# Optimization experiments

Hardware: AMD Instinct MI355X
Metric: run time of the kernel (lower is better)

## Reference

```python
import jax, jax.numpy as jnp
import numpy as np

N_USER = 50000
N_ITEM = 50000
N_EDGE = 1600000
D_IN = 64
D_OUT = 64


def _mean_agg(msgs, dst, num_dst):
    # copy_u + mean: segment-mean of edge messages onto dst nodes; zero for
    # zero-in-degree nodes (DGL default).
    s = jax.ops.segment_sum(msgs, dst, num_segments=num_dst)          # [Nd, D]
    cnt = jax.ops.segment_sum(jnp.ones((msgs.shape[0],), msgs.dtype), dst,
                              num_segments=num_dst)                    # [Nd]
    return s / jnp.maximum(cnt, 1.0)[:, None]


def setup_inputs() -> dict:
    key = jax.random.key(0)
    ks = jax.random.split(key, 12)
    return {
        'user_feat': jax.random.normal(ks[0], (N_USER, D_IN), jnp.float32),
        'item_feat': jax.random.normal(ks[1], (N_ITEM, D_IN), jnp.float32),
        'rate_src': jax.random.randint(ks[2], (N_EDGE,), 0, N_USER, jnp.int64 if jax.config.jax_enable_x64 else jnp.int32),
        'rate_dst': jax.random.randint(ks[3], (N_EDGE,), 0, N_ITEM, jnp.int64 if jax.config.jax_enable_x64 else jnp.int32),
        'rev_src': jax.random.randint(ks[4], (N_EDGE,), 0, N_ITEM, jnp.int64 if jax.config.jax_enable_x64 else jnp.int32),
        'rev_dst': jax.random.randint(ks[5], (N_EDGE,), 0, N_USER, jnp.int64 if jax.config.jax_enable_x64 else jnp.int32),
        'W_rate': jax.random.normal(ks[6], (D_IN, D_OUT), jnp.float32) * (1.0 / np.sqrt(D_IN)),
        'b_rate': jnp.zeros((D_OUT,), jnp.float32),
        'W_rev': jax.random.normal(ks[7], (D_IN, D_OUT), jnp.float32) * (1.0 / np.sqrt(D_IN)),
        'b_rev': jnp.zeros((D_OUT,), jnp.float32),
        'loop_weight': jax.random.normal(ks[8], (D_IN, D_OUT), jnp.float32) * (1.0 / np.sqrt(D_IN)),
        'h_bias': jnp.zeros((D_OUT,), jnp.float32),
    }


def reference(user_feat, item_feat, rate_src, rate_dst, rev_src, rev_dst,
              W_rate, b_rate, W_rev, b_rev, loop_weight, h_bias):
    # Per-etype Linear on source-node features (applied node-wise, as in torch).
    Wh_rate = user_feat @ W_rate + b_rate      # [Nu, Dout], etype 'rate': user->item
    Wh_rev = item_feat @ W_rev + b_rev         # [Ni, Dout], etype 'rated-by': item->user

    # copy_u + mean per etype, cross-reduce 'sum' (one etype per dst ntype here).
    h_item = _mean_agg(Wh_rate[rate_src], rate_dst, N_ITEM)
    h_user = _mean_agg(Wh_rev[rev_src], rev_dst, N_USER)

    # self-loop + bias (dropout p=0.0 is identity)
    h_user = h_user + user_feat @ loop_weight + h_bias
    h_item = h_item + item_feat @ loop_weight + h_bias
    return (h_user, h_item)
```

## Files before the change

### kernel.cpp

```cpp
#include <hip/hip_runtime.h>

#define N_USER 50000
#define N_ITEM 50000
#define N_NODE 50000
#define N_EDGE 1600000
#define D 64

#define FB_SHIFT 7
#define N_FINE 400
#define CAP 5120
#define BIN_CHUNK 2048
#define NCAST 3125
#define NBIN ((N_EDGE + BIN_CHUNK - 1) / BIN_CHUNK)

typedef __attribute__((ext_vector_type(8))) short short8;
typedef __attribute__((ext_vector_type(4))) float floatx4;

__device__ __forceinline__ unsigned short f32_to_bf16(float x) {
    unsigned u = __float_as_uint(x);
    unsigned r = (u + 0x7FFFu + ((u >> 16) & 1u)) >> 16;
    return (unsigned short)r;
}
__device__ __forceinline__ float bf16_to_f32(unsigned short h) {
    return __uint_as_float(((unsigned)h) << 16);
}

__global__ __launch_bounds__(256) void cast_bin(
    const float4* __restrict__ fU, ushort4* __restrict__ bU,
    const float4* __restrict__ fI, ushort4* __restrict__ bI,
    const int* __restrict__ srcA, const int* __restrict__ dstA, unsigned* __restrict__ binA,
    const int* __restrict__ srcB, const int* __restrict__ dstB, unsigned* __restrict__ binB,
    int* __restrict__ fcur)
{
    __shared__ int hist[N_FINE];
    __shared__ int lcur[N_FINE];
    const int id = blockIdx.x;

    if (id >= 2 * NBIN) {
        const int cid = id - 2 * NBIN;
        const int et = (cid >= NCAST) ? 1 : 0;
        const float4* __restrict__ in = et ? fI : fU;
        ushort4* __restrict__ out     = et ? bI : bU;
        int i = (cid - et * NCAST) * 256 + threadIdx.x;
        float4 v = in[i];
        ushort4 o;
        o.x = f32_to_bf16(v.x); o.y = f32_to_bf16(v.y);
        o.z = f32_to_bf16(v.z); o.w = f32_to_bf16(v.w);
        out[i] = o;
        return;
    }

    const int et = (id >= NBIN) ? 1 : 0;
    const int chunk = id - et * NBIN;
    const int* __restrict__ src = et ? srcB : srcA;
    const int* __restrict__ dst = et ? dstB : dstA;
    unsigned* __restrict__ bin  = et ? binB : binA;
    int* __restrict__ fc = fcur + et * N_FINE;

    for (int i = threadIdx.x; i < N_FINE; i += 256) hist[i] = 0;
    __syncthreads();

    const int base = chunk * BIN_CHUNK;
    const int n4 = (min(BIN_CHUNK, N_EDGE - base)) >> 2;
    const int4* dst4 = (const int4*)(dst + base);
    const int4* src4 = (const int4*)(src + base);

    for (int i = threadIdx.x; i < n4; i += 256) {
        int4 d = dst4[i];
        atomicAdd(&hist[d.x >> FB_SHIFT], 1);
        atomicAdd(&hist[d.y >> FB_SHIFT], 1);
        atomicAdd(&hist[d.z >> FB_SHIFT], 1);
        atomicAdd(&hist[d.w >> FB_SHIFT], 1);
    }
    __syncthreads();
    for (int f = threadIdx.x; f < N_FINE; f += 256) {
        int c = hist[f];
        lcur[f] = c ? (f * CAP + atomicAdd(&fc[f], c)) : 0;
    }
    __syncthreads();
    for (int i = threadIdx.x; i < n4; i += 256) {
        int4 d = dst4[i];
        int4 s = src4[i];
        { int pos = atomicAdd(&lcur[d.x >> FB_SHIFT], 1); bin[pos] = ((unsigned)d.x << 16) | (unsigned)s.x; }
        { int pos = atomicAdd(&lcur[d.y >> FB_SHIFT], 1); bin[pos] = ((unsigned)d.y << 16) | (unsigned)s.y; }
        { int pos = atomicAdd(&lcur[d.z >> FB_SHIFT], 1); bin[pos] = ((unsigned)d.z << 16) | (unsigned)s.z; }
        { int pos = atomicAdd(&lcur[d.w >> FB_SHIFT], 1); bin[pos] = ((unsigned)d.w << 16) | (unsigned)s.w; }
    }
}

__global__ __launch_bounds__(256) void bucket_sort(
    const unsigned* __restrict__ binI, unsigned short* __restrict__ srtI,
    int* __restrict__ offI, int* __restrict__ cntI,
    const unsigned* __restrict__ binU, unsigned short* __restrict__ srtU,
    int* __restrict__ offU, int* __restrict__ cntU,
    const int* __restrict__ fcur)
{
    const int et = blockIdx.y;
    const unsigned* __restrict__ bin = et ? binU : binI;
    unsigned short* __restrict__ srt = et ? srtU : srtI;
    int* __restrict__ off  = et ? offU : offI;
    int* __restrict__ cntG = et ? cntU : cntI;
    const int f = blockIdx.x;
    const int start = f * CAP;
    const int end   = start + fcur[et * N_FINE + f];
    const int nodebase = f << FB_SHIFT;

    __shared__ int cnt[128];
    __shared__ int sc[128];
    __shared__ int pos[128];
    if (threadIdx.x < 128) cnt[threadIdx.x] = 0;
    __syncthreads();

    for (int e = start + threadIdx.x; e < end; e += 256) {
        int ld = (int)(bin[e] >> 16) - nodebase;
        atomicAdd(&cnt[ld], 1);
    }
    __syncthreads();

    if (threadIdx.x < 128) sc[threadIdx.x] = cnt[threadIdx.x];
    __syncthreads();
    for (int o = 1; o < 128; o <<= 1) {
        int t = 0;
        if (threadIdx.x < 128 && threadIdx.x >= o) t = sc[threadIdx.x - o];
        __syncthreads();
        if (threadIdx.x < 128) sc[threadIdx.x] += t;
        __syncthreads();
    }
    if (threadIdx.x < 128) {
        int base = start + sc[threadIdx.x] - cnt[threadIdx.x];
        pos[threadIdx.x] = base;
        int node = nodebase + threadIdx.x;
        if (node < N_NODE) { off[node] = base; cntG[node] = cnt[threadIdx.x]; }
    }
    __syncthreads();

    for (int e = start + threadIdx.x; e < end; e += 256) {
        unsigned p = bin[e];
        int ld = (int)(p >> 16) - nodebase;
        int q = atomicAdd(&pos[ld], 1);
        srt[q] = (unsigned short)(p & 0xFFFFu);
    }
}

__global__ __launch_bounds__(256) void aggregate_kernel(
    const ushort4* __restrict__ itemB,
    const ushort4* __restrict__ userB,
    const int* __restrict__ offU, const int* __restrict__ cntU, const unsigned short* __restrict__ srtU,
    const int* __restrict__ offI, const int* __restrict__ cntI, const unsigned short* __restrict__ srtI,
    ushort4* __restrict__ aggU, ushort4* __restrict__ aggI)
{
    int g = blockIdx.x * 16 + (threadIdx.x >> 4);
    if (g >= N_USER + N_ITEM) return;
    const int lane = threadIdx.x & 15;

    const bool isUser = (g < N_USER);
    const int d = isUser ? g : g - N_USER;
    const ushort4* __restrict__ tab = isUser ? itemB : userB;
    const int* __restrict__ off     = isUser ? offU : offI;
    const int* __restrict__ cntG    = isUser ? cntU : cntI;
    const unsigned short* __restrict__ srt = isUser ? srtU : srtI;
    ushort4* __restrict__ agg       = isUser ? aggU : aggI;

    const int start = off[d];
    const int c     = cntG[d];
    const int end   = start + c;

    float4 a0 = make_float4(0.f, 0.f, 0.f, 0.f);
    float4 a1 = make_float4(0.f, 0.f, 0.f, 0.f);
    float4 a2 = make_float4(0.f, 0.f, 0.f, 0.f);
    float4 a3 = make_float4(0.f, 0.f, 0.f, 0.f);
    int e = start;
    for (; e + 4 <= end; e += 4) {
        int s0 = (int)srt[e],     s1 = (int)srt[e + 1];
        int s2 = (int)srt[e + 2], s3 = (int)srt[e + 3];
        ushort4 w0 = tab[(size_t)s0 * 16 + lane];
        ushort4 w1 = tab[(size_t)s1 * 16 + lane];
        ushort4 w2 = tab[(size_t)s2 * 16 + lane];
        ushort4 w3 = tab[(size_t)s3 * 16 + lane];
        a0.x += bf16_to_f32(w0.x); a0.y += bf16_to_f32(w0.y);
        a0.z += bf16_to_f32(w0.z); a0.w += bf16_to_f32(w0.w);
        a1.x += bf16_to_f32(w1.x); a1.y += bf16_to_f32(w1.y);
        a1.z += bf16_to_f32(w1.z); a1.w += bf16_to_f32(w1.w);
        a2.x += bf16_to_f32(w2.x); a2.y += bf16_to_f32(w2.y);
        a2.z += bf16_to_f32(w2.z); a2.w += bf16_to_f32(w2.w);
        a3.x += bf16_to_f32(w3.x); a3.y += bf16_to_f32(w3.y);
        a3.z += bf16_to_f32(w3.z); a3.w += bf16_to_f32(w3.w);
    }
    for (; e < end; ++e) {
        int s0 = (int)srt[e];
        ushort4 w0 = tab[(size_t)s0 * 16 + lane];
        a0.x += bf16_to_f32(w0.x); a0.y += bf16_to_f32(w0.y);
        a0.z += bf16_to_f32(w0.z); a0.w += bf16_to_f32(w0.w);
    }
    a0.x += a1.x + a2.x + a3.x;
    a0.y += a1.y + a2.y + a3.y;
    a0.z += a1.z + a2.z + a3.z;
    a0.w += a1.w + a2.w + a3.w;

    const float inv = (c > 0) ? 1.0f / (float)c : 0.0f;
    ushort4 o;
    o.x = f32_to_bf16(a0.x * inv);
    o.y = f32_to_bf16(a0.y * inv);
    o.z = f32_to_bf16(a0.z * inv);
    o.w = f32_to_bf16(a0.w * inv);
    agg[(size_t)g * 16 + lane - (isUser ? 0 : (size_t)N_USER * 16)] = o;
}

__global__ __launch_bounds__(256, 4) void final_gemm(
    const unsigned short* __restrict__ aggU_, const unsigned short* __restrict__ featU_,
    const int* __restrict__ cntU_, const float* __restrict__ WU,
    const float* __restrict__ beU,
    const unsigned short* __restrict__ aggI_, const unsigned short* __restrict__ featI_,
    const int* __restrict__ cntI_, const float* __restrict__ WI,
    const float* __restrict__ beI,
    const float* __restrict__ loop_w, const float* __restrict__ h_bias,
    float* __restrict__ out)
{
    const int et = blockIdx.y;
    const unsigned short* __restrict__ agg  = et ? aggI_ : aggU_;
    const unsigned short* __restrict__ feat = et ? featI_ : featU_;
    const int* __restrict__ cntG            = et ? cntI_ : cntU_;
    const float* __restrict__ W             = et ? WI : WU;
    const float* __restrict__ b_et          = et ? beI : beU;
    float* __restrict__ outN = out + (et ? (size_t)N_USER * D : 0);

    __shared__ unsigned short sWt[64][72];
    __shared__ unsigned short sLt[64][72];
    __shared__ float sbe[64], sbh[64];
    __shared__ int sCnt[64];

    const int tid = threadIdx.x;
    const int row0 = blockIdx.x * 64;

    for (int i = tid; i < 4096; i += 256) {
        int k = i >> 6, n = i & 63;
        sWt[n][k] = f32_to_bf16(W[i]);
        sLt[n][k] = f32_to_bf16(loop_w[i]);
    }
    if (tid < 64) {
        sbe[tid] = b_et[tid];
        sbh[tid] = h_bias[tid];
        int r = row0 + tid;
        sCnt[tid] = (r < N_NODE) ? cntG[r] : 0;
    }
    __syncthreads();

    const int wave = tid >> 6;
    const int lane = tid & 63;
    const int quad = lane >> 4;
    const int l16  = lane & 15;

    const int rowA = row0 + wave * 16 + l16;
    const int rA = (rowA < N_NODE) ? rowA : (N_NODE - 1);
    short8 aAgg0  = *(const short8*)(agg  + (size_t)rA * 64 +      quad * 8);
    short8 aAgg1  = *(const short8*)(agg  + (size_t)rA * 64 + 32 + quad * 8);
    short8 aFeat0 = *(const short8*)(feat + (size_t)rA * 64 +      quad * 8);
    short8 aFeat1 = *(const short8*)(feat + (size_t)rA * 64 + 32 + quad * 8);

    floatx4 acc[4];
    #pragma unroll
    for (int t = 0; t < 4; ++t) {
        const int n = t * 16 + l16;
        short8 bW0 = *(const short8*)&sWt[n][     quad * 8];
        short8 bW1 = *(const short8*)&sWt[n][32 + quad * 8];
        short8 bL0 = *(const short8*)&sLt[n][     quad * 8];
        short8 bL1 = *(const short8*)&sLt[n][32 + quad * 8];
        floatx4 a = {0.f, 0.f, 0.f, 0.f};
        a = __builtin_amdgcn_mfma_f32_16x16x32_bf16(aAgg0,  bW0, a, 0, 0, 0);
        a = __builtin_amdgcn_mfma_f32_16x16x32_bf16(aAgg1,  bW1, a, 0, 0, 0);
        a = __builtin_amdgcn_mfma_f32_16x16x32_bf16(aFeat0, bL0, a, 0, 0, 0);
        a = __builtin_amdgcn_mfma_f32_16x16x32_bf16(aFeat1, bL1, a, 0, 0, 0);
        acc[t] = a;
    }

    #pragma unroll
    for (int t = 0; t < 4; ++t) {
        const int col = t * 16 + l16;
        const float bh = sbh[col], be = sbe[col];
        #pragma unroll
        for (int i = 0; i < 4; ++i) {
            int lrow = wave * 16 + quad * 4 + i;
            int r = row0 + lrow;
            if (r < N_NODE) {
                float v = acc[t][i] + bh + (sCnt[lrow] > 0 ? be : 0.f);
                outN[(size_t)r * D + col] = v;
            }
        }
    }
}

extern "C" void kernel_launch(void* const* d_in, const int* in_sizes, int n_in,
                              void* d_out, int out_size, void* d_ws, size_t ws_size,
                              hipStream_t stream)
{
    const float* user_feat = (const float*)d_in[0];
    const float* item_feat = (const float*)d_in[1];
    const int*   rate_src  = (const int*)d_in[2];
    const int*   rate_dst  = (const int*)d_in[3];
    const int*   rev_src   = (const int*)d_in[4];
    const int*   rev_dst   = (const int*)d_in[5];
    const float* W_rate    = (const float*)d_in[6];
    const float* b_rate    = (const float*)d_in[7];
    const float* W_rev     = (const float*)d_in[8];
    const float* b_rev     = (const float*)d_in[9];
    const float* loop_w    = (const float*)d_in[10];
    const float* h_bias    = (const float*)d_in[11];
    float* out = (float*)d_out;

    char* p = (char*)d_ws;
    ushort4* userB = (ushort4*)p; p += (size_t)N_USER * D * 2;
    ushort4* itemB = (ushort4*)p; p += (size_t)N_ITEM * D * 2;
    unsigned* binI = (unsigned*)p; p += (size_t)N_FINE * CAP * 4;
    unsigned* binU = (unsigned*)p; p += (size_t)N_FINE * CAP * 4;
    unsigned short* srtI = (unsigned short*)p; p += (size_t)N_FINE * CAP * 2;
    unsigned short* srtU = (unsigned short*)p; p += (size_t)N_FINE * CAP * 2;
    ushort4* aggI  = (ushort4*)p; p += (size_t)N_NODE * D * 2;
    ushort4* aggU  = (ushort4*)p; p += (size_t)N_NODE * D * 2;
    int* offI = (int*)p; p += (size_t)N_NODE * 4;
    int* offU = (int*)p; p += (size_t)N_NODE * 4;
    int* cntI = (int*)p; p += (size_t)N_NODE * 4;
    int* cntU = (int*)p; p += (size_t)N_NODE * 4;
    int* fcur = (int*)p; p += (size_t)(2 * N_FINE) * 4;
    (void)ws_size;

    hipMemsetAsync(fcur, 0, (size_t)(2 * N_FINE) * sizeof(int), stream);

    cast_bin<<<dim3(2 * NBIN + 2 * NCAST), 256, 0, stream>>>(
        (const float4*)user_feat, userB, (const float4*)item_feat, itemB,
        rate_src, rate_dst, binI,
        rev_src,  rev_dst,  binU, fcur);

    bucket_sort<<<dim3(N_FINE, 2), 256, 0, stream>>>(
        binI, srtI, offI, cntI,
        binU, srtU, offU, cntU, fcur);

    aggregate_kernel<<<(N_USER + N_ITEM + 15) / 16, 256, 0, stream>>>(
        itemB, userB,
        offU, cntU, srtU,
        offI, cntI, srtI,
        aggU, aggI);

    final_gemm<<<dim3((N_NODE + 63) / 64, 2), 256, 0, stream>>>(
        (const unsigned short*)aggU, (const unsigned short*)userB, cntU, W_rev, b_rev,
        (const unsigned short*)aggI, (const unsigned short*)itemB, cntI, W_rate, b_rate,
        loop_w, h_bias, out);

    (void)in_sizes; (void)n_in; (void)out_size;
}
```

Before: 233.3 us.

## Replace two-level bucket sort with global histogram, scan, and atomic scatter CSR build

Replaces the coarse-bin plus per-bucket sort with a direct CSR build. A global atomic histogram on dst is fused with the bf16 cast, then a single-block-per-etype scan produces offsets, then an atomic scatter writes source ids into their final positions. This drops the intermediate packed bin array and its second pass, but adds a serial-ish two-block scan kernel and global atomics on 50k counters, which scatter writes randomly.

```diff
diff --git a/kernel.cpp b/kernel.cpp
--- a/kernel.cpp
+++ b/kernel.cpp
@@ -6,12 +6,12 @@
 #define N_EDGE 1600000
 #define D 64
 
-#define FB_SHIFT 7
-#define N_FINE 400
-#define CAP 5120
-#define BIN_CHUNK 2048
 #define NCAST 3125
-#define NBIN ((N_EDGE + BIN_CHUNK - 1) / BIN_CHUNK)
+#define HCHUNK 8192
+#define NH ((N_EDGE + HCHUNK - 1) / HCHUNK)
+#define SCHUNK 4096
+#define NSC ((N_EDGE + SCHUNK - 1) / SCHUNK)
+#define SCAN_C 49
 
 typedef __attribute__((ext_vector_type(8))) short short8;
 typedef __attribute__((ext_vector_type(4))) float floatx4;
@@ -25,19 +25,16 @@
     return __uint_as_float(((unsigned)h) << 16);
 }
 
-__global__ __launch_bounds__(256) void cast_bin(
+__global__ __launch_bounds__(256) void hist_cast(
     const float4* __restrict__ fU, ushort4* __restrict__ bU,
     const float4* __restrict__ fI, ushort4* __restrict__ bI,
-    const int* __restrict__ srcA, const int* __restrict__ dstA, unsigned* __restrict__ binA,
-    const int* __restrict__ srcB, const int* __restrict__ dstB, unsigned* __restrict__ binB,
-    int* __restrict__ fcur)
-{
-    __shared__ int hist[N_FINE];
-    __shared__ int lcur[N_FINE];
+    const int* __restrict__ dstA, int* __restrict__ cntI_,
+    const int* __restrict__ dstB, int* __restrict__ cntU_)
+{
     const int id = blockIdx.x;
 
-    if (id >= 2 * NBIN) {
-        const int cid = id - 2 * NBIN;
+    if (id >= 2 * NH) {
+        const int cid = id - 2 * NH;
         const int et = (cid >= NCAST) ? 1 : 0;
         const float4* __restrict__ in = et ? fI : fU;
         ushort4* __restrict__ out     = et ? bI : bU;
@@ -50,95 +47,88 @@
         return;
     }
 
-    const int et = (id >= NBIN) ? 1 : 0;
-    const int chunk = id - et * NBIN;
+    const int et = (id >= NH) ? 1 : 0;
+    const int* __restrict__ dst = et ? dstB : dstA;
+    int* __restrict__ cnt       = et ? cntU_ : cntI_;
+    const int base = (id - et * NH) * HCHUNK;
+    const int n4 = (min(HCHUNK, N_EDGE - base)) >> 2;
+    const int4* dst4 = (const int4*)(dst + base);
+    for (int i = threadIdx.x; i < n4; i += 256) {
+        int4 d = dst4[i];
+        atomicAdd(&cnt[d.x], 1);
+        atomicAdd(&cnt[d.y], 1);
+        atomicAdd(&cnt[d.z], 1);
+        atomicAdd(&cnt[d.w], 1);
+    }
+}
+
+__global__ __launch_bounds__(1024) void scan_kernel(
+    const int* __restrict__ cntI_, int* __restrict__ offI, int* __restrict__ curI,
+    const int* __restrict__ cntU_, int* __restrict__ offU, int* __restrict__ curU)
+{
+    const int et = blockIdx.x;
+    const int* __restrict__ cnt = et ? cntU_ : cntI_;
+    int* __restrict__ off       = et ? offU : offI;
+    int* __restrict__ cur       = et ? curU : curI;
+
+    __shared__ int part[1024];
+    const int t = threadIdx.x;
+    const int base = t * SCAN_C;
+
+    int sum = 0;
+    for (int i = 0; i < SCAN_C; ++i) {
+        int idx = base + i;
+        sum += (idx < N_NODE) ? cnt[idx] : 0;
+    }
+    part[t] = sum;
+    __syncthreads();
+
+    for (int o = 1; o < 1024; o <<= 1) {
+        int v = (t >= o) ? part[t - o] : 0;
+        __syncthreads();
+        part[t] += v;
+        __syncthreads();
+    }
+
+    int run = part[t] - sum;
+    for (int i = 0; i < SCAN_C; ++i) {
+        int idx = base + i;
+        if (idx < N_NODE) {
+            off[idx] = run;
+            cur[idx] = run;
+            run += cnt[idx];
+        }
+    }
+}
+
+__global__ __launch_bounds__(256) void scatter_kernel(
+    const int* __restrict__ srcA, const int* __restrict__ dstA,
+    int* __restrict__ curI, unsigned short* __restrict__ srtI,
+    const int* __restrict__ srcB, const int* __restrict__ dstB,
+    int* __restrict__ curU, unsigned short* __restrict__ srtU)
+{
+    const int et = blockIdx.y;
     const int* __restrict__ src = et ? srcB : srcA;
     const int* __restrict__ dst = et ? dstB : dstA;
-    unsigned* __restrict__ bin  = et ? binB : binA;
-    int* __restrict__ fc = fcur + et * N_FINE;
-
-    for (int i = threadIdx.x; i < N_FINE; i += 256) hist[i] = 0;
-    __syncthreads();
-
-    const int base = chunk * BIN_CHUNK;
-    const int n4 = (min(BIN_CHUNK, N_EDGE - base)) >> 2;
+    int* __restrict__ cur       = et ? curU : curI;
+    unsigned short* __restrict__ srt = et ? srtU : srtI;
+
+    const int base = blockIdx.x * SCHUNK;
+    const int n4 = (min(SCHUNK, N_EDGE - base)) >> 2;
     const int4* dst4 = (const int4*)(dst + base);
     const int4* src4 = (const int4*)(src + base);
 
-    for (int i = threadIdx.x; i < n4; i += 256) {
-        int4 d = dst4[i];
-        atomicAdd(&hist[d.x >> FB_SHIFT], 1);
-        atomicAdd(&hist[d.y >> FB_SHIFT], 1);
-        atomicAdd(&hist[d.z >> FB_SHIFT], 1);
-        atomicAdd(&hist[d.w >> FB_SHIFT], 1);
-    }
-    __syncthreads();
-    for (int f = threadIdx.x; f < N_FINE; f += 256) {
-        int c = hist[f];
-        lcur[f] = c ? (f * CAP + atomicAdd(&fc[f], c)) : 0;
-    }
-    __syncthreads();
     for (int i = threadIdx.x; i < n4; i += 256) {
         int4 d = dst4[i];
         int4 s = src4[i];
-        { int pos = atomicAdd(&lcur[d.x >> FB_SHIFT], 1); bin[pos] = ((unsigned)d.x << 16) | (unsigned)s.x; }
-        { int pos = atomicAdd(&lcur[d.y >> FB_SHIFT], 1); bin[pos] = ((unsigned)d.y << 16) | (unsigned)s.y; }
-        { int pos = atomicAdd(&lcur[d.z >> FB_SHIFT], 1); bin[pos] = ((unsigned)d.z << 16) | (unsigned)s.z; }
-        { int pos = atomicAdd(&lcur[d.w >> FB_SHIFT], 1); bin[pos] = ((unsigned)d.w << 16) | (unsigned)s.w; }
-    }
-}
-
-__global__ __launch_bounds__(256) void bucket_sort(
-    const unsigned* __restrict__ binI, unsigned short* __restrict__ srtI,
-    int* __restrict__ offI, int* __restrict__ cntI,
-    const unsigned* __restrict__ binU, unsigned short* __restrict__ srtU,
-    int* __restrict__ offU, int* __restrict__ cntU,
-    const int* __restrict__ fcur)
-{
-    const int et = blockIdx.y;
-    const unsigned* __restrict__ bin = et ? binU : binI;
-    unsigned short* __restrict__ srt = et ? srtU : srtI;
-    int* __restrict__ off  = et ? offU : offI;
-    int* __restrict__ cntG = et ? cntU : cntI;
-    const int f = blockIdx.x;
-    const int start = f * CAP;
-    const int end   = start + fcur[et * N_FINE + f];
-    const int nodebase = f << FB_SHIFT;
-
-    __shared__ int cnt[128];
-    __shared__ int sc[128];
-    __shared__ int pos[128];
-    if (threadIdx.x < 128) cnt[threadIdx.x] = 0;
-    __syncthreads();
-
-    for (int e = start + threadIdx.x; e < end; e += 256) {
-        int ld = (int)(bin[e] >> 16) - nodebase;
-        atomicAdd(&cnt[ld], 1);
-    }
-    __syncthreads();
-
-    if (threadIdx.x < 128) sc[threadIdx.x] = cnt[threadIdx.x];
-    __syncthreads();
-    for (int o = 1; o < 128; o <<= 1) {
-        int t = 0;
-        if (threadIdx.x < 128 && threadIdx.x >= o) t = sc[threadIdx.x - o];
-        __syncthreads();
-        if (threadIdx.x < 128) sc[threadIdx.x] += t;
-        __syncthreads();
-    }
-    if (threadIdx.x < 128) {
-        int base = start + sc[threadIdx.x] - cnt[threadIdx.x];
-        pos[threadIdx.x] = base;
-        int node = nodebase + threadIdx.x;
-        if (node < N_NODE) { off[node] = base; cntG[node] = cnt[threadIdx.x]; }
-    }
-    __syncthreads();
-
-    for (int e = start + threadIdx.x; e < end; e += 256) {
-        unsigned p = bin[e];
-        int ld = (int)(p >> 16) - nodebase;
-        int q = atomicAdd(&pos[ld], 1);
-        srt[q] = (unsigned short)(p & 0xFFFFu);
+        int p0 = atomicAdd(&cur[d.x], 1);
+        int p1 = atomicAdd(&cur[d.y], 1);
+        int p2 = atomicAdd(&cur[d.z], 1);
+        int p3 = atomicAdd(&cur[d.w], 1);
+        srt[p0] = (unsigned short)s.x;
+        srt[p1] = (unsigned short)s.y;
+        srt[p2] = (unsigned short)s.z;
+        srt[p3] = (unsigned short)s.w;
     }
 }
 
@@ -310,29 +300,32 @@
     char* p = (char*)d_ws;
     ushort4* userB = (ushort4*)p; p += (size_t)N_USER * D * 2;
     ushort4* itemB = (ushort4*)p; p += (size_t)N_ITEM * D * 2;
-    unsigned* binI = (unsigned*)p; p += (size_t)N_FINE * CAP * 4;
-    unsigned* binU = (unsigned*)p; p += (size_t)N_FINE * CAP * 4;
-    unsigned short* srtI = (unsigned short*)p; p += (size_t)N_FINE * CAP * 2;
-    unsigned short* srtU = (unsigned short*)p; p += (size_t)N_FINE * CAP * 2;
+    unsigned short* srtI = (unsigned short*)p; p += (size_t)N_EDGE * 2;
+    unsigned short* srtU = (unsigned short*)p; p += (size_t)N_EDGE * 2;
     ushort4* aggI  = (ushort4*)p; p += (size_t)N_NODE * D * 2;
     ushort4* aggU  = (ushort4*)p; p += (size_t)N_NODE * D * 2;
+    int* cntI = (int*)p; p += (size_t)N_NODE * 4;
+    int* cntU = (int*)p; p += (size_t)N_NODE * 4;
     int* offI = (int*)p; p += (size_t)N_NODE * 4;
     int* offU = (int*)p; p += (size_t)N_NODE * 4;
-    int* cntI = (int*)p; p += (size_t)N_NODE * 4;
-    int* cntU = (int*)p; p += (size_t)N_NODE * 4;
-    int* fcur = (int*)p; p += (size_t)(2 * N_FINE) * 4;
+    int* curI = (int*)p; p += (size_t)N_NODE * 4;
+    int* curU = (int*)p; p += (size_t)N_NODE * 4;
     (void)ws_size;
 
-    hipMemsetAsync(fcur, 0, (size_t)(2 * N_FINE) * sizeof(int), stream);
-
-    cast_bin<<<dim3(2 * NBIN + 2 * NCAST), 256, 0, stream>>>(
+    hipMemsetAsync(cntI, 0, (size_t)2 * N_NODE * sizeof(int), stream);
+
+    hist_cast<<<dim3(2 * NH + 2 * NCAST), 256, 0, stream>>>(
         (const float4*)user_feat, userB, (const float4*)item_feat, itemB,
-        rate_src, rate_dst, binI,
-        rev_src,  rev_dst,  binU, fcur);
-
-    bucket_sort<<<dim3(N_FINE, 2), 256, 0, stream>>>(
-        binI, srtI, offI, cntI,
-        binU, srtU, offU, cntU, fcur);
+        rate_dst, cntI,
+        rev_dst,  cntU);
+
+    scan_kernel<<<dim3(2), 1024, 0, stream>>>(
+        cntI, offI, curI,
+        cntU, offU, curU);
+
+    scatter_kernel<<<dim3(NSC, 2), 256, 0, stream>>>(
+        rate_src, rate_dst, curI, srtI,
+        rev_src,  rev_dst,  curU, srtU);
 
     aggregate_kernel<<<(N_USER + N_ITEM + 15) / 16, 256, 0, stream>>>(
         itemB, userB,
```

After: 667.0 us. 186% more time.

## Stage edge binning in shared memory and coarsen buckets for coalesced writes

Applied to the files above, without the earlier changes.

The binning kernel now sorts each 8192-edge chunk locally in LDS by coarse bucket (256 nodes) and then writes each bucket's run contiguously to global memory, instead of scattering individual edges straight to global positions. Bucket sort likewise builds its sorted source array in LDS and writes it out coalesced, using fewer, larger buckets (196 × 10240). This targets scattered global writes, at the cost of about 32KB of LDS per binning block and larger shared arrays in the sort kernel. Those LDS sizes lower occupancy, and the cast blocks in the same kernel also allocate the LDS array.

```diff
diff --git a/kernel.cpp b/kernel.cpp
--- a/kernel.cpp
+++ b/kernel.cpp
@@ -6,12 +6,12 @@
 #define N_EDGE 1600000
 #define D 64
 
-#define FB_SHIFT 7
-#define N_FINE 400
-#define CAP 5120
-#define BIN_CHUNK 2048
+#define CB_SHIFT 8
+#define NBKT 196
+#define BCAP 10240
+#define CHUNK 8192
+#define NCH ((N_EDGE + CHUNK - 1) / CHUNK)
 #define NCAST 3125
-#define NBIN ((N_EDGE + BIN_CHUNK - 1) / BIN_CHUNK)
 
 typedef __attribute__((ext_vector_type(8))) short short8;
 typedef __attribute__((ext_vector_type(4))) float floatx4;
@@ -28,16 +28,21 @@
 __global__ __launch_bounds__(256) void cast_bin(
     const float4* __restrict__ fU, ushort4* __restrict__ bU,
     const float4* __restrict__ fI, ushort4* __restrict__ bI,
-    const int* __restrict__ srcA, const int* __restrict__ dstA, unsigned* __restrict__ binA,
-    const int* __restrict__ srcB, const int* __restrict__ dstB, unsigned* __restrict__ binB,
+    const int* __restrict__ srcA, const int* __restrict__ dstA, unsigned* __restrict__ gbinA,
+    const int* __restrict__ srcB, const int* __restrict__ dstB, unsigned* __restrict__ gbinB,
     int* __restrict__ fcur)
 {
-    __shared__ int hist[N_FINE];
-    __shared__ int lcur[N_FINE];
+    __shared__ unsigned lbin[CHUNK];
+    __shared__ int hist[NBKT];
+    __shared__ int lofs[NBKT];
+    __shared__ int lcur[NBKT];
+    __shared__ int gbase[NBKT];
+    __shared__ int sc[256];
+
     const int id = blockIdx.x;
 
-    if (id >= 2 * NBIN) {
-        const int cid = id - 2 * NBIN;
+    if (id >= 2 * NCH) {
+        const int cid = id - 2 * NCH;
         const int et = (cid >= NCAST) ? 1 : 0;
         const float4* __restrict__ in = et ? fI : fU;
         ushort4* __restrict__ out     = et ? bI : bU;
@@ -50,96 +55,121 @@
         return;
     }
 
-    const int et = (id >= NBIN) ? 1 : 0;
-    const int chunk = id - et * NBIN;
+    const int et = (id >= NCH) ? 1 : 0;
+    const int chunk = id - et * NCH;
     const int* __restrict__ src = et ? srcB : srcA;
     const int* __restrict__ dst = et ? dstB : dstA;
-    unsigned* __restrict__ bin  = et ? binB : binA;
-    int* __restrict__ fc = fcur + et * N_FINE;
-
-    for (int i = threadIdx.x; i < N_FINE; i += 256) hist[i] = 0;
-    __syncthreads();
-
-    const int base = chunk * BIN_CHUNK;
-    const int n4 = (min(BIN_CHUNK, N_EDGE - base)) >> 2;
+    unsigned* __restrict__ gbin = et ? gbinB : gbinA;
+    int* __restrict__ fc = fcur + et * NBKT;
+
+    const int base = chunk * CHUNK;
+    const int nE = min(CHUNK, N_EDGE - base);
+    const int n4 = nE >> 2;
     const int4* dst4 = (const int4*)(dst + base);
     const int4* src4 = (const int4*)(src + base);
-
-    for (int i = threadIdx.x; i < n4; i += 256) {
+    const int tid = threadIdx.x;
+
+    for (int i = tid; i < NBKT; i += 256) hist[i] = 0;
+    __syncthreads();
+
+    for (int i = tid; i < n4; i += 256) {
         int4 d = dst4[i];
-        atomicAdd(&hist[d.x >> FB_SHIFT], 1);
-        atomicAdd(&hist[d.y >> FB_SHIFT], 1);
-        atomicAdd(&hist[d.z >> FB_SHIFT], 1);
-        atomicAdd(&hist[d.w >> FB_SHIFT], 1);
-    }
-    __syncthreads();
-    for (int f = threadIdx.x; f < N_FINE; f += 256) {
-        int c = hist[f];
-        lcur[f] = c ? (f * CAP + atomicAdd(&fc[f], c)) : 0;
-    }
-    __syncthreads();
-    for (int i = threadIdx.x; i < n4; i += 256) {
+        atomicAdd(&hist[d.x >> CB_SHIFT], 1);
+        atomicAdd(&hist[d.y >> CB_SHIFT], 1);
+        atomicAdd(&hist[d.z >> CB_SHIFT], 1);
+        atomicAdd(&hist[d.w >> CB_SHIFT], 1);
+    }
+    __syncthreads();
+
+    int v = (tid < NBKT) ? hist[tid] : 0;
+    sc[tid] = v;
+    __syncthreads();
+    for (int o = 1; o < 256; o <<= 1) {
+        int t = (tid >= o) ? sc[tid - o] : 0;
+        __syncthreads();
+        sc[tid] += t;
+        __syncthreads();
+    }
+    if (tid < NBKT) {
+        int excl = sc[tid] - v;
+        lofs[tid] = excl;
+        lcur[tid] = excl;
+        gbase[tid] = v ? (tid * BCAP + atomicAdd(&fc[tid], v)) : 0;
+    }
+    __syncthreads();
+
+    for (int i = tid; i < n4; i += 256) {
         int4 d = dst4[i];
         int4 s = src4[i];
-        { int pos = atomicAdd(&lcur[d.x >> FB_SHIFT], 1); bin[pos] = ((unsigned)d.x << 16) | (unsigned)s.x; }
-        { int pos = atomicAdd(&lcur[d.y >> FB_SHIFT], 1); bin[pos] = ((unsigned)d.y << 16) | (unsigned)s.y; }
-        { int pos = atomicAdd(&lcur[d.z >> FB_SHIFT], 1); bin[pos] = ((unsigned)d.z << 16) | (unsigned)s.z; }
-        { int pos = atomicAdd(&lcur[d.w >> FB_SHIFT], 1); bin[pos] = ((unsigned)d.w << 16) | (unsigned)s.w; }
+        { int p = atomicAdd(&lcur[d.x >> CB_SHIFT], 1); lbin[p] = ((unsigned)d.x << 16) | (unsigned)s.x; }
+        { int p = atomicAdd(&lcur[d.y >> CB_SHIFT], 1); lbin[p] = ((unsigned)d.y << 16) | (unsigned)s.y; }
+        { int p = atomicAdd(&lcur[d.z >> CB_SHIFT], 1); lbin[p] = ((unsigned)d.z << 16) | (unsigned)s.z; }
+        { int p = atomicAdd(&lcur[d.w >> CB_SHIFT], 1); lbin[p] = ((unsigned)d.w << 16) | (unsigned)s.w; }
+    }
+    __syncthreads();
+
+    const int wv = tid >> 6, ln = tid & 63;
+    for (int b = wv; b < NBKT; b += 4) {
+        const int s0 = lofs[b], c = hist[b], g = gbase[b];
+        for (int t = ln; t < c; t += 64) gbin[g + t] = lbin[s0 + t];
     }
 }
 
 __global__ __launch_bounds__(256) void bucket_sort(
-    const unsigned* __restrict__ binI, unsigned short* __restrict__ srtI,
+    const unsigned* __restrict__ gbinI, unsigned short* __restrict__ srtI,
     int* __restrict__ offI, int* __restrict__ cntI,
-    const unsigned* __restrict__ binU, unsigned short* __restrict__ srtU,
+    const unsigned* __restrict__ gbinU, unsigned short* __restrict__ srtU,
     int* __restrict__ offU, int* __restrict__ cntU,
     const int* __restrict__ fcur)
 {
     const int et = blockIdx.y;
-    const unsigned* __restrict__ bin = et ? binU : binI;
-    unsigned short* __restrict__ srt = et ? srtU : srtI;
-    int* __restrict__ off  = et ? offU : offI;
-    int* __restrict__ cntG = et ? cntU : cntI;
-    const int f = blockIdx.x;
-    const int start = f * CAP;
-    const int end   = start + fcur[et * N_FINE + f];
-    const int nodebase = f << FB_SHIFT;
-
-    __shared__ int cnt[128];
-    __shared__ int sc[128];
-    __shared__ int pos[128];
-    if (threadIdx.x < 128) cnt[threadIdx.x] = 0;
-    __syncthreads();
-
-    for (int e = start + threadIdx.x; e < end; e += 256) {
-        int ld = (int)(bin[e] >> 16) - nodebase;
-        atomicAdd(&cnt[ld], 1);
-    }
-    __syncthreads();
-
-    if (threadIdx.x < 128) sc[threadIdx.x] = cnt[threadIdx.x];
-    __syncthreads();
-    for (int o = 1; o < 128; o <<= 1) {
-        int t = 0;
-        if (threadIdx.x < 128 && threadIdx.x >= o) t = sc[threadIdx.x - o];
+    const unsigned* __restrict__ gbin = et ? gbinU : gbinI;
+    unsigned short* __restrict__ srt  = et ? srtU : srtI;
+    int* __restrict__ off   = et ? offU : offI;
+    int* __restrict__ cntG  = et ? cntU : cntI;
+    const int b = blockIdx.x;
+    const int startg = b * BCAP;
+    const int n = fcur[et * NBKT + b];
+    const int nodebase = b << CB_SHIFT;
+    const int tid = threadIdx.x;
+
+    __shared__ int cnt[256];
+    __shared__ int sc[256];
+    __shared__ int pos[256];
+    __shared__ unsigned short lsrt[BCAP];
+
+    cnt[tid] = 0;
+    __syncthreads();
+
+    for (int i = tid; i < n; i += 256)
+        atomicAdd(&cnt[(int)(gbin[startg + i] >> 16) - nodebase], 1);
+    __syncthreads();
+
+    int v = cnt[tid];
+    sc[tid] = v;
+    __syncthreads();
+    for (int o = 1; o < 256; o <<= 1) {
+        int t = (tid >= o) ? sc[tid - o] : 0;
         __syncthreads();
-        if (threadIdx.x < 128) sc[threadIdx.x] += t;
+        sc[tid] += t;
         __syncthreads();
     }
-    if (threadIdx.x < 128) {
-        int base = start + sc[threadIdx.x] - cnt[threadIdx.x];
-        pos[threadIdx.x] = base;
-        int node = nodebase + threadIdx.x;
-        if (node < N_NODE) { off[node] = base; cntG[node] = cnt[threadIdx.x]; }
-    }
-    __syncthreads();
-
-    for (int e = start + threadIdx.x; e < end; e += 256) {
-        unsigned p = bin[e];
-        int ld = (int)(p >> 16) - nodebase;
-        int q = atomicAdd(&pos[ld], 1);
-        srt[q] = (unsigned short)(p & 0xFFFFu);
-    }
+    {
+        int excl = sc[tid] - v;
+        pos[tid] = excl;
+        int node = nodebase + tid;
+        if (node < N_NODE) { off[node] = startg + excl; cntG[node] = v; }
+    }
+    __syncthreads();
+
+    for (int i = tid; i < n; i += 256) {
+        unsigned p = gbin[startg + i];
+        int q = atomicAdd(&pos[(int)(p >> 16) - nodebase], 1);
+        lsrt[q] = (unsigned short)(p & 0xFFFFu);
+    }
+    __syncthreads();
+
+    for (int i = tid; i < n; i += 256) srt[startg + i] = lsrt[i];
 }
 
 __global__ __launch_bounds__(256) void aggregate_kernel(
@@ -310,29 +340,29 @@
     char* p = (char*)d_ws;
     ushort4* userB = (ushort4*)p; p += (size_t)N_USER * D * 2;
     ushort4* itemB = (ushort4*)p; p += (size_t)N_ITEM * D * 2;
-    unsigned* binI = (unsigned*)p; p += (size_t)N_FINE * CAP * 4;
-    unsigned* binU = (unsigned*)p; p += (size_t)N_FINE * CAP * 4;
-    unsigned short* srtI = (unsigned short*)p; p += (size_t)N_FINE * CAP * 2;
-    unsigned short* srtU = (unsigned short*)p; p += (size_t)N_FINE * CAP * 2;
+    unsigned* gbinI = (unsigned*)p; p += (size_t)NBKT * BCAP * 4;
+    unsigned* gbinU = (unsigned*)p; p += (size_t)NBKT * BCAP * 4;
+    unsigned short* srtI = (unsigned short*)p; p += (size_t)NBKT * BCAP * 2;
+    unsigned short* srtU = (unsigned short*)p; p += (size_t)NBKT * BCAP * 2;
     ushort4* aggI  = (ushort4*)p; p += (size_t)N_NODE * D * 2;
     ushort4* aggU  = (ushort4*)p; p += (size_t)N_NODE * D * 2;
     int* offI = (int*)p; p += (size_t)N_NODE * 4;
     int* offU = (int*)p; p += (size_t)N_NODE * 4;
     int* cntI = (int*)p; p += (size_t)N_NODE * 4;
     int* cntU = (int*)p; p += (size_t)N_NODE * 4;
-    int* fcur = (int*)p; p += (size_t)(2 * N_FINE) * 4;
+    int* fcur = (int*)p; p += (size_t)(2 * NBKT) * 4;
     (void)ws_size;
 
-    hipMemsetAsync(fcur, 0, (size_t)(2 * N_FINE) * sizeof(int), stream);
-
-    cast_bin<<<dim3(2 * NBIN + 2 * NCAST), 256, 0, stream>>>(
+    hipMemsetAsync(fcur, 0, (size_t)(2 * NBKT) * sizeof(int), stream);
+
+    cast_bin<<<dim3(2 * NCH + 2 * NCAST), 256, 0, stream>>>(
         (const float4*)user_feat, userB, (const float4*)item_feat, itemB,
-        rate_src, rate_dst, binI,
-        rev_src,  rev_dst,  binU, fcur);
-
-    bucket_sort<<<dim3(N_FINE, 2), 256, 0, stream>>>(
-        binI, srtI, offI, cntI,
-        binU, srtU, offU, cntU, fcur);
+        rate_src, rate_dst, gbinI,
+        rev_src,  rev_dst,  gbinU, fcur);
+
+    bucket_sort<<<dim3(NBKT, 2), 256, 0, stream>>>(
+        gbinI, srtI, offI, cntI,
+        gbinU, srtU, offU, cntU, fcur);
 
     aggregate_kernel<<<(N_USER + N_ITEM + 15) / 16, 256, 0, stream>>>(
         itemB, userB,
```

New measurement: 208.8 us. 10.5% less time.
